# Kernel tuning notes

Hardware: AMD Instinct MI355X
Metric: run time of the kernel (lower is better)

## Reference

```python
import jax, jax.numpy as jnp
import numpy as np

B, H, W = 4, 128, 128
THRESHOLD = 0.1      # hard-coded in chamfer_distance_batch
CHUNK = 2048         # row-chunk size for the online-min over the distance matrix
BIG = 1e9            # masks out inactive columns in the min-reduction
EMPTY_CHD = 1e6      # sentinel when either point set is empty (matches torch code)
EPS = 1e-12          # sqrt clamp for numerical safety


def setup_inputs() -> dict:
    key = jax.random.key(0)
    k1, k2 = jax.random.split(key)
    batch1 = jax.random.normal(k1, (B, H, W), dtype=jnp.float32)
    batch2 = jax.random.normal(k2, (B, H, W), dtype=jnp.float32)
    return {"batch1": batch1, "batch2": batch2}


def _chamfer(batch1, batch2):
    Bn, Hn, Wn = batch1.shape
    HW = Hn * Wn
    w1 = jax.nn.relu(batch1 - THRESHOLD).reshape(Bn, HW)   # [B, HW]
    w2 = jax.nn.relu(batch2 - THRESHOLD).reshape(Bn, HW)
    gy, gx = jnp.meshgrid(jnp.arange(Hn), jnp.arange(Wn), indexing='ij')
    coords = jnp.stack([gy, gx], axis=-1).reshape(HW, 2).astype(jnp.float32)  # [HW, 2]
    # torch code multiplies coords by the relu'd weights BEFORE cdist (quirk kept)
    c1 = coords[None, :, :] * w1[:, :, None]               # [B, HW, 2]
    c2 = coords[None, :, :] * w2[:, :, None]
    m1 = w1 > 0                                            # active-point masks
    m2 = w2 > 0

    def directed(cf, mf, ct, mt):
        # mean over active rows of min distance to active columns, chunked
        ct_sq = jnp.sum(ct * ct, axis=-1)                  # [HW]

        def chunk_min(cc):                                 # cc: [CHUNK, 2]
            # |a-b|^2 = |a|^2 + |b|^2 - 2 a.b  (GEMM form)
            d2 = (jnp.sum(cc * cc, axis=-1)[:, None]
                  + ct_sq[None, :]
                  - 2.0 * cc @ ct.T)                       # [CHUNK, HW]
            d = jnp.sqrt(jnp.maximum(d2, EPS))
            return jnp.min(jnp.where(mt[None, :], d, BIG), axis=1)  # [CHUNK]

        mins = jax.lax.map(chunk_min, cf.reshape(-1, CHUNK, 2)).reshape(-1)  # [HW]
        n = jnp.sum(mf)
        return jnp.sum(mins * mf) / jnp.maximum(n, 1)

    def per_image(c1b, m1b, c2b, m2b):
        chd = directed(c1b, m1b, c2b, m2b) + directed(c2b, m2b, c1b, m1b)
        nonempty = (jnp.sum(m1b) > 0) & (jnp.sum(m2b) > 0)
        return jnp.where(nonempty, chd, jnp.asarray(EMPTY_CHD, chd.dtype))

    return jax.vmap(per_image)(c1, m1, c2, m2)   # [B]


def reference(batch1, batch2):
    return _chamfer(batch1, batch2)
```

## Files before the change

kernel.cpp:

```cpp
#include <hip/hip_runtime.h>
#include <math.h>


#define B_ 4
#define HW_ 16384
#define THRESH 0.1f
#define BIGF 1e30f
#define EPS_ 1e-12f

#define SEGCAP 4096
#define NSEG 4
#define NBIN 256
#define BINSCALE 0.25f
#define BINW 4.0f
#define RG 128
#define NW 4
#define AWIN 1024
#define PD_NGRP 128

__global__ __launch_bounds__(1024)
void compact_kernel(const float* __restrict__ in1, const float* __restrict__ in2,
                    int* __restrict__ segcounts, float4* __restrict__ pts,
                    uint4* __restrict__ minarr4, int* __restrict__ histG) {
    int seg = blockIdx.x, combo = blockIdx.y;
    int b = combo >> 1, s = combo & 1;
    int tid = threadIdx.x, lane = tid & 63, wid = tid >> 6;
    const float* in = s ? in2 : in1;
    int ibase = seg * SEGCAP + tid * 4;
    float4 v = ((const float4*)(in + b * HW_))[(unsigned)ibase >> 2];
    float w0 = v.x - THRESH, w1 = v.y - THRESH, w2 = v.z - THRESH, w3 = v.w - THRESH;
    int a0 = w0 > 0.f, a1 = w1 > 0.f, a2 = w2 > 0.f, a3 = w3 > 0.f;

    unsigned int bb = __float_as_uint(BIGF);
    minarr4[(unsigned)(combo * HW_ + ibase) >> 2] = make_uint4(bb, bb, bb, bb);

    __shared__ int hist[NBIN];
    if (tid < NBIN) hist[tid] = 0;

    int c = a0 + a1 + a2 + a3;
    int incl = c;
#pragma unroll
    for (int o = 1; o < 64; o <<= 1) {
        int x = __shfl_up(incl, o, 64);
        if (lane >= o) incl += x;
    }
    int wexcl = incl - c;
    __shared__ int wtot[16], wpre[17];
    if (lane == 63) wtot[wid] = incl;
    __syncthreads();
    if (tid == 0) {
        int run = 0;
#pragma unroll
        for (int ww = 0; ww < 16; ++ww) { wpre[ww] = run; run += wtot[ww]; }
        wpre[16] = run;
    }
    __syncthreads();
    int off = wpre[wid] + wexcl;
    float4* dst = pts + combo * HW_ + seg * SEGCAP;
    float wv[4] = {w0, w1, w2, w3};
    int   av[4] = {a0, a1, a2, a3};
#pragma unroll
    for (int u = 0; u < 4; ++u) {
        if (av[u]) {
            int i = ibase + u;
            float qx = (float)(i >> 7) * wv[u];
            float qy = (float)(i & 127) * wv[u];
            float zz = qx * qx + qy * qy;
            dst[off] = make_float4(qx, qy, zz, 0.0f);
            int bin = min(NBIN - 1, (int)(sqrtf(zz) * BINSCALE));
            atomicAdd(&hist[bin], 1);
            ++off;
        }
    }
    if (tid == 0) segcounts[combo * 4 + seg] = wpre[16];
    __syncthreads();
    if (tid < NBIN)
        histG[(combo * NSEG + seg) * NBIN + tid] = hist[tid];
}

__global__ __launch_bounds__(512)
void scatter_kernel(const int* __restrict__ segcounts, const float4* __restrict__ pts,
                    const int* __restrict__ histG, float4* __restrict__ sorted,
                    int* __restrict__ binstartG) {
    int seg = blockIdx.x, combo = blockIdx.y;
    int tid = threadIdx.x;
    __shared__ int h[NSEG][NBIN];
    __shared__ int sc[NBIN];
    __shared__ int cur[NBIN];
    for (int i = tid; i < NSEG * NBIN; i += 512)
        h[i >> 8][i & 255] = histG[combo * NSEG * NBIN + i];
    __syncthreads();
    if (tid < NBIN) sc[tid] = h[0][tid] + h[1][tid] + h[2][tid] + h[3][tid];
    __syncthreads();
#pragma unroll
    for (int o = 1; o < NBIN; o <<= 1) {
        int v = (tid < NBIN && tid >= o) ? sc[tid - o] : 0;
        __syncthreads();
        if (tid < NBIN) sc[tid] += v;
        __syncthreads();
    }
    if (tid < NBIN) {
        int tot = h[0][tid] + h[1][tid] + h[2][tid] + h[3][tid];
        int excl = sc[tid] - tot;
        int o2 = excl;
        for (int s2 = 0; s2 < seg; ++s2) o2 += h[s2][tid];
        cur[tid] = o2;
        if (seg == 0) binstartG[combo * (NBIN + 1) + tid] = excl;
    }
    if (seg == 0 && tid == 0)
        binstartG[combo * (NBIN + 1) + NBIN] = sc[NBIN - 1];
    __syncthreads();
    int c = segcounts[combo * 4 + seg];
    const float4* src = pts + combo * HW_ + seg * SEGCAP;
    for (int i = tid; i < c; i += 512) {
        float4 p = src[i];
        int bin = min(NBIN - 1, (int)(sqrtf(p.z) * BINSCALE));
        int idx = atomicAdd(&cur[bin], 1);
        sorted[(size_t)combo * HW_ + idx] =
            make_float4(p.x, p.y, p.z, __uint_as_float((unsigned)(seg * SEGCAP + i)));
    }
}

__global__ __launch_bounds__(256)
void pdist_kernel(const float4* __restrict__ sorted, const int* __restrict__ binstart,
                  unsigned int* __restrict__ minarr) {
    int grp = blockIdx.x, combo = blockIdx.y;
    int tid = threadIdx.x, lane = tid & 63, w = tid >> 6;
    int tc = combo ^ 1;
    int n_from = binstart[combo * (NBIN + 1) + NBIN];
    int n_to   = binstart[tc * (NBIN + 1) + NBIN];
    if (n_from <= 0 || n_to <= 0) return;
    int rbase = grp * RG;
    if (rbase >= n_from) return;

    const float4* __restrict__ rows = sorted + (size_t)combo * HW_;
    const float4* __restrict__ cols = sorted + (size_t)tc * HW_;

    int r0 = rbase + lane, r1 = rbase + 64 + lane;
    bool v0 = r0 < n_from, v1 = r1 < n_from;
    float4 P0 = rows[min(r0, n_from - 1)];
    float4 P1 = rows[min(r1, n_from - 1)];
    float npx0 = -2.0f * P0.x, npy0 = -2.0f * P0.y, p20 = P0.z;
    float npx1 = -2.0f * P1.x, npy1 = -2.0f * P1.y, p21 = P1.z;
    unsigned int slot0 = __float_as_uint(P0.w);
    unsigned int slot1 = __float_as_uint(P1.w);
    float m0 = BIGF, m1 = BIGF;

    int blo_r = min(NBIN - 1, (int)(sqrtf(rows[rbase].z) * BINSCALE));
    int bhi_r = min(NBIN - 1, (int)(sqrtf(rows[min(rbase + RG - 1, n_from - 1)].z) * BINSCALE));
    float rho_lo = (float)blo_r * BINW;
    float rho_hi = (float)(bhi_r + 1) * BINW;

    int jmid = min(binstart[tc * (NBIN + 1) + blo_r], n_to);
    int aHi = min(n_to, jmid + AWIN / 2);
    int aLo = max(0, aHi - AWIN);
    aHi = min(n_to, aLo + AWIN);

    __shared__ __align__(16) float bx[NW][64], by[NW][64], bz[NW][64];
    __shared__ float mW[NW][RG];

    auto batch = [&](int jb) {
        int j = jb + lane;
        float4 q = (j < n_to) ? cols[j] : make_float4(0.0f, 0.0f, BIGF, 0.0f);
        bx[w][lane] = q.x; by[w][lane] = q.y; bz[w][lane] = q.z;
        const float4* X = (const float4*)bx[w];
        const float4* Y = (const float4*)by[w];
        const float4* Z = (const float4*)bz[w];
#pragma unroll
        for (int q4 = 0; q4 < 16; ++q4) {
            float4 qx = X[q4], qy = Y[q4], qz = Z[q4];
            float t0 = fmaf(qy.x, npy0, fmaf(qx.x, npx0, qz.x));
            float u1 = fmaf(qy.y, npy0, fmaf(qx.y, npx0, qz.y));
            m0 = fminf(m0, fminf(t0, u1));
            float u2 = fmaf(qy.z, npy0, fmaf(qx.z, npx0, qz.z));
            float u3 = fmaf(qy.w, npy0, fmaf(qx.w, npx0, qz.w));
            m0 = fminf(m0, fminf(u2, u3));
            float s0 = fmaf(qy.x, npy1, fmaf(qx.x, npx1, qz.x));
            float s1 = fmaf(qy.y, npy1, fmaf(qx.y, npx1, qz.y));
            m1 = fminf(m1, fminf(s0, s1));
            float s2 = fmaf(qy.z, npy1, fmaf(qx.z, npx1, qz.z));
            float s3 = fmaf(qy.w, npy1, fmaf(qx.w, npx1, qz.w));
            m1 = fminf(m1, fminf(s2, s3));
        }
    };

    int nbA = (aHi - aLo + 63) >> 6;
    for (int bi = w; bi < nbA; bi += NW) batch(aLo + (bi << 6));

    mW[w][lane] = m0; mW[w][64 + lane] = m1;
    __syncthreads();
    float c0 = fminf(fminf(mW[0][lane], mW[1][lane]),
                     fminf(mW[2][lane], mW[3][lane]));
    float c1 = fminf(fminf(mW[0][64 + lane], mW[1][64 + lane]),
                     fminf(mW[2][64 + lane], mW[3][64 + lane]));
    float md0 = v0 ? fmaxf(c0 + p20, 0.0f) : -1.0f;
    float md1 = v1 ? fmaxf(c1 + p21, 0.0f) : -1.0f;
    float g = fmaxf(md0, md1);
#pragma unroll
    for (int o = 1; o < 64; o <<= 1) g = fmaxf(g, __shfl_xor(g, o));

    float S = sqrtf((g + 1.0f) * (1.0f / 0.99f)) * 1.001f;
    int b_lo = max(0, (int)((rho_lo - S) * BINSCALE) - 1);
    int b_hi = min(NBIN, (int)((rho_hi + S) * BINSCALE) + 2);
    int jlo2 = binstart[tc * (NBIN + 1) + b_lo];
    int jhi2 = binstart[tc * (NBIN + 1) + b_hi];

    m0 = c0; m1 = c1;
    int nbL = (max(0, aLo - jlo2) + 63) >> 6;
    int nbR = (max(0, jhi2 - aHi) + 63) >> 6;
    for (int bi = w; bi < nbL + nbR; bi += NW) {
        int jb = (bi < nbL) ? (jlo2 + (bi << 6)) : (aHi + ((bi - nbL) << 6));
        batch(jb);
    }
    __syncthreads();
    mW[w][lane] = m0; mW[w][64 + lane] = m1;
    __syncthreads();
    if (w == 0) {
        float f0 = fminf(fminf(mW[0][lane], mW[1][lane]),
                         fminf(mW[2][lane], mW[3][lane]));
        float f1 = fminf(fminf(mW[0][64 + lane], mW[1][64 + lane]),
                         fminf(mW[2][64 + lane], mW[3][64 + lane]));
        if (v0) minarr[combo * HW_ + slot0] = __float_as_uint(fmaxf(f0 + p20, 0.0f));
        if (v1) minarr[combo * HW_ + slot1] = __float_as_uint(fmaxf(f1 + p21, 0.0f));
    }
}

__global__ void reduce_out_kernel(const int* __restrict__ segcounts,
                                  const unsigned int* __restrict__ minarr,
                                  float* __restrict__ out) {
    int b = blockIdx.x;
    int tid = threadIdx.x;
    int d = tid >> 9;
    int t = tid & 511;
    int combo = b * 2 + d;

    float acc = 0.0f;
    for (int s = 0; s < NSEG; ++s) {
        int c = segcounts[combo * 4 + s];
        const unsigned int* ma = minarr + combo * HW_ + s * SEGCAP;
        for (int r = t; r < c; r += 512)
            acc += sqrtf(fmaxf(__uint_as_float(ma[r]), EPS_));
    }
#pragma unroll
    for (int o = 32; o >= 1; o >>= 1) acc += __shfl_down(acc, o);

    __shared__ float wsum[16];
    if ((tid & 63) == 0) wsum[tid >> 6] = acc;
    __syncthreads();
    if (tid == 0) {
        float s0 = 0.0f, s1 = 0.0f;
#pragma unroll
        for (int w = 0; w < 8; ++w)  s0 += wsum[w];
#pragma unroll
        for (int w = 8; w < 16; ++w) s1 += wsum[w];
        int n0 = 0, n1 = 0;
#pragma unroll
        for (int s = 0; s < NSEG; ++s) {
            n0 += segcounts[(b * 2) * 4 + s];
            n1 += segcounts[(b * 2 + 1) * 4 + s];
        }
        out[b] = (n0 > 0 && n1 > 0)
                 ? s0 / (float)n0 + s1 / (float)n1
                 : 1.0e6f;
    }
}

extern "C" void kernel_launch(void* const* d_in, const int* in_sizes, int n_in,
                              void* d_out, int out_size, void* d_ws, size_t ws_size,
                              hipStream_t stream) {
    const float* in1 = (const float*)d_in[0];
    const float* in2 = (const float*)d_in[1];
    float* out = (float*)d_out;
    char* ws = (char*)d_ws;
    int* segcounts = (int*)ws;
    float4* pts = (float4*)(ws + 256);
    size_t minoff = 256 + (size_t)8 * HW_ * sizeof(float4);
    unsigned int* minarr = (unsigned int*)(ws + minoff);
    size_t sortoff = minoff + (size_t)8 * HW_ * sizeof(unsigned int);
    float4* sorted = (float4*)(ws + sortoff);
    size_t binoff = sortoff + (size_t)8 * HW_ * sizeof(float4);
    int* binstart = (int*)(ws + binoff);
    size_t histoff = binoff + (size_t)8 * (NBIN + 1) * sizeof(int);
    int* histG = (int*)(ws + histoff);

    hipLaunchKernelGGL(compact_kernel, dim3(NSEG, 8), dim3(1024), 0, stream,
                       in1, in2, segcounts, pts, (uint4*)minarr, histG);
    hipLaunchKernelGGL(scatter_kernel, dim3(NSEG, 8), dim3(512), 0, stream,
                       segcounts, pts, histG, sorted, binstart);
    hipLaunchKernelGGL(pdist_kernel, dim3(PD_NGRP, 8), dim3(256), 0, stream,
                       sorted, binstart, minarr);
    hipLaunchKernelGGL(reduce_out_kernel, dim3(B_), dim3(1024), 0, stream,
                       segcounts, minarr, out);
}
```

Before: 88.71 us.

## Double wavefronts per pdist block, prefetch column batches, and center approximation window

The pdist kernel now runs 8 wavefronts per block instead of 4, so each row group's column scan is split across more waves. The global load of the next column batch is issued before the current one is processed, hiding memory latency behind the FMA/min work. The initial approximate window is also centered between the row group's low and high bins rather than anchored at the low bin, which should give a tighter first bound and a narrower second pass. The costs are more shared memory, a longer cross-wave min reduction, and higher register pressure from the prefetch under launch_bounds(512,4).

```diff
diff --git a/kernel.cpp b/kernel.cpp
--- a/kernel.cpp
+++ b/kernel.cpp
@@ -14,7 +14,7 @@
 #define BINSCALE 0.25f
 #define BINW 4.0f
 #define RG 128
-#define NW 4
+#define NW 8
 #define AWIN 1024
 #define PD_NGRP 128
 
@@ -121,7 +121,7 @@
     }
 }
 
-__global__ __launch_bounds__(256)
+__global__ __launch_bounds__(512, 4)
 void pdist_kernel(const float4* __restrict__ sorted, const int* __restrict__ binstart,
                   unsigned int* __restrict__ minarr) {
     int grp = blockIdx.x, combo = blockIdx.y;
@@ -151,7 +151,8 @@
     float rho_lo = (float)blo_r * BINW;
     float rho_hi = (float)(bhi_r + 1) * BINW;
 
-    int jmid = min(binstart[tc * (NBIN + 1) + blo_r], n_to);
+    int jmid = (binstart[tc * (NBIN + 1) + blo_r]
+                + binstart[tc * (NBIN + 1) + min(bhi_r + 1, NBIN)]) >> 1;
     int aHi = min(n_to, jmid + AWIN / 2);
     int aLo = max(0, aHi - AWIN);
     aHi = min(n_to, aLo + AWIN);
@@ -159,10 +160,12 @@
     __shared__ __align__(16) float bx[NW][64], by[NW][64], bz[NW][64];
     __shared__ float mW[NW][RG];
 
-    auto batch = [&](int jb) {
+    auto ld = [&](int jb) -> float4 {
         int j = jb + lane;
-        float4 q = (j < n_to) ? cols[j] : make_float4(0.0f, 0.0f, BIGF, 0.0f);
-        bx[w][lane] = q.x; by[w][lane] = q.y; bz[w][lane] = q.z;
+        return (j < n_to) ? cols[j] : make_float4(0.0f, 0.0f, BIGF, 0.0f);
+    };
+    auto proc = [&](float4 qc) {
+        bx[w][lane] = qc.x; by[w][lane] = qc.y; bz[w][lane] = qc.z;
         const float4* X = (const float4*)bx[w];
         const float4* Y = (const float4*)by[w];
         const float4* Z = (const float4*)bz[w];
@@ -185,14 +188,22 @@
     };
 
     int nbA = (aHi - aLo + 63) >> 6;
-    for (int bi = w; bi < nbA; bi += NW) batch(aLo + (bi << 6));
+    float4 qn = (w < nbA) ? ld(aLo + (w << 6))
+                          : make_float4(0.0f, 0.0f, BIGF, 0.0f);
+    for (int bi = w; bi < nbA; bi += NW) {
+        float4 qc = qn;
+        if (bi + NW < nbA) qn = ld(aLo + ((bi + NW) << 6));
+        proc(qc);
+    }
 
     mW[w][lane] = m0; mW[w][64 + lane] = m1;
     __syncthreads();
-    float c0 = fminf(fminf(mW[0][lane], mW[1][lane]),
-                     fminf(mW[2][lane], mW[3][lane]));
-    float c1 = fminf(fminf(mW[0][64 + lane], mW[1][64 + lane]),
-                     fminf(mW[2][64 + lane], mW[3][64 + lane]));
+    float c0 = mW[0][lane], c1 = mW[0][64 + lane];
+#pragma unroll
+    for (int ww = 1; ww < NW; ++ww) {
+        c0 = fminf(c0, mW[ww][lane]);
+        c1 = fminf(c1, mW[ww][64 + lane]);
+    }
     float md0 = v0 ? fmaxf(c0 + p20, 0.0f) : -1.0f;
     float md1 = v1 ? fmaxf(c1 + p21, 0.0f) : -1.0f;
     float g = fmaxf(md0, md1);
@@ -208,18 +219,26 @@
     m0 = c0; m1 = c1;
     int nbL = (max(0, aLo - jlo2) + 63) >> 6;
     int nbR = (max(0, jhi2 - aHi) + 63) >> 6;
-    for (int bi = w; bi < nbL + nbR; bi += NW) {
-        int jb = (bi < nbL) ? (jlo2 + (bi << 6)) : (aHi + ((bi - nbL) << 6));
-        batch(jb);
+    int nbB = nbL + nbR;
+    auto jbB = [&](int bi) {
+        return (bi < nbL) ? (jlo2 + (bi << 6)) : (aHi + ((bi - nbL) << 6));
+    };
+    qn = (w < nbB) ? ld(jbB(w)) : make_float4(0.0f, 0.0f, BIGF, 0.0f);
+    for (int bi = w; bi < nbB; bi += NW) {
+        float4 qc = qn;
+        if (bi + NW < nbB) qn = ld(jbB(bi + NW));
+        proc(qc);
     }
     __syncthreads();
     mW[w][lane] = m0; mW[w][64 + lane] = m1;
     __syncthreads();
     if (w == 0) {
-        float f0 = fminf(fminf(mW[0][lane], mW[1][lane]),
-                         fminf(mW[2][lane], mW[3][lane]));
-        float f1 = fminf(fminf(mW[0][64 + lane], mW[1][64 + lane]),
-                         fminf(mW[2][64 + lane], mW[3][64 + lane]));
+        float f0 = mW[0][lane], f1 = mW[0][64 + lane];
+#pragma unroll
+        for (int ww = 1; ww < NW; ++ww) {
+            f0 = fminf(f0, mW[ww][lane]);
+            f1 = fminf(f1, mW[ww][64 + lane]);
+        }
         if (v0) minarr[combo * HW_ + slot0] = __float_as_uint(fmaxf(f0 + p20, 0.0f));
         if (v1) minarr[combo * HW_ + slot1] = __float_as_uint(fmaxf(f1 + p21, 0.0f));
     }
@@ -287,7 +306,7 @@
                        in1, in2, segcounts, pts, (uint4*)minarr, histG);
     hipLaunchKernelGGL(scatter_kernel, dim3(NSEG, 8), dim3(512), 0, stream,
                        segcounts, pts, histG, sorted, binstart);
-    hipLaunchKernelGGL(pdist_kernel, dim3(PD_NGRP, 8), dim3(256), 0, stream,
+    hipLaunchKernelGGL(pdist_kernel, dim3(PD_NGRP, 8), dim3(512), 0, stream,
                        sorted, binstart, minarr);
     hipLaunchKernelGGL(reduce_out_kernel, dim3(B_), dim3(1024), 0, stream,
                        segcounts, minarr, out);
```

Result: faster. 83.69 us (-5.7%).
